# Optimization experiments

Hardware: AMD Instinct MI355X
Metric: run time of the kernel (lower is better)

Reference implementation:

```python
import jax, jax.numpy as jnp
import numpy as np

W = 192      # image width (seq len for attn1)
HN = 192     # H * N (seq len for attn2)
C = 128      # hidden_dim
NHEAD = 8


def setup_inputs() -> dict:
    key = jax.random.key(0)
    ks = jax.random.split(key, 12)
    sc = 0.05  # small init so softmax is well-conditioned
    feat = jax.random.normal(ks[0], (W, 2 * HN, C), jnp.float32)
    pos = jax.random.normal(ks[1], (2 * W - 1, C), jnp.float32)
    pos_y = jax.random.normal(ks[2], (2 * HN - 1, C), jnp.float32)
    i = jnp.arange(W)
    pos_indexes = (i[:, None] - i[None, :] + W - 1).reshape(-1).astype(jnp.int32)
    j = jnp.arange(HN)
    pos_indexes_y = (j[:, None] - j[None, :] + HN - 1).reshape(-1).astype(jnp.int32)
    return {
        "feat": feat,
        "pos": pos,
        "pos_y": pos_y,
        "ln_w": jnp.ones((C,), jnp.float32),
        "ln_b": jnp.zeros((C,), jnp.float32),
        "w_in1": jax.random.normal(ks[3], (3 * C, C), jnp.float32) * sc,
        "b_in1": jnp.zeros((3 * C,), jnp.float32),
        "w_out1": jax.random.normal(ks[4], (C, C), jnp.float32) * sc,
        "b_out1": jnp.zeros((C,), jnp.float32),
        "w_in2": jax.random.normal(ks[5], (3 * C, C), jnp.float32) * sc,
        "b_in2": jnp.zeros((3 * C,), jnp.float32),
        "w_out2": jax.random.normal(ks[6], (C, C), jnp.float32) * sc,
        "b_out2": jnp.zeros((C,), jnp.float32),
        "pos_indexes": pos_indexes,
        "pos_indexes_y": pos_indexes_y,
    }


def _layernorm(x, g, b, eps=1e-5):
    m = x.mean(-1, keepdims=True)
    v = ((x - m) ** 2).mean(-1, keepdims=True)
    return (x - m) / jnp.sqrt(v + eps) * g + b


def _rel_attn(x, pos_enc, pos_idx, w_in, b_in, w_out, b_out):
    # x: [w, bsz, c]; pos_enc: [2w-1, c]; pos_idx: [w*w]
    w, bsz, c = x.shape
    hd = c // NHEAD
    scale = float(hd) ** -0.5
    q, k, v = jnp.split(x @ w_in.T + b_in, 3, axis=-1)
    pe = pos_enc[pos_idx].reshape(w, w, c)           # [w, w, c] relative pos
    q_r, k_r = jnp.split(pe @ w_in[: 2 * c].T + b_in[: 2 * c], 2, axis=-1)
    q = (q * scale).reshape(w, bsz, NHEAD, hd)
    k = k.reshape(w, bsz, NHEAD, hd)
    v = v.reshape(w, bsz, NHEAD, hd)
    q_r = (q_r * scale).reshape(w, w, NHEAD, hd)
    k_r = k_r.reshape(w, w, NHEAD, hd)
    # content-content + content-pos + pos-content -> [bsz, nhead, w, w]
    attn = (jnp.einsum('wnec,vnec->newv', q, k)
            + jnp.einsum('wnec,wvec->newv', q, k_r)
            + jnp.einsum('vnec,wvec->newv', k, q_r))
    attn = jax.nn.softmax(attn, axis=-1)
    out = jnp.einsum('newv,vnec->wnec', attn, v).reshape(w, bsz, c)
    return out @ w_out.T + b_out


def reference(feat, pos, pos_y, ln_w, ln_b,
              w_in1, b_in1, w_out1, b_out1,
              w_in2, b_in2, w_out2, b_out2,
              pos_indexes, pos_indexes_y):
    w, h2, c = feat.shape
    f2 = _layernorm(feat, ln_w, ln_b)
    # [W, 2HN, C] -> [HN, 2W, C]: attention along vertical (H) axis
    f2 = f2.reshape(w, 2, h2 // 2, c).transpose(2, 1, 0, 3).reshape(h2 // 2, 2 * w, c)
    f2 = _rel_attn(f2, pos_y, pos_indexes_y, w_in2, b_in2, w_out2, b_out2)
    # back to [W, 2HN, C]: attention along horizontal (W) axis
    f2 = f2.reshape(h2 // 2, 2, w, c).transpose(2, 1, 0, 3).reshape(w, h2, c)
    f2 = _rel_attn(f2, pos, pos_indexes, w_in1, b_in1, w_out1, b_out1)
    return feat + f2
```

## Files before the change

kernel.cpp:

```cpp
#include <hip/hip_runtime.h>
#include <hip/hip_bf16.h>


typedef unsigned short u16;
typedef short bf16x8 __attribute__((ext_vector_type(8)));
typedef float f32x4 __attribute__((ext_vector_type(4)));
typedef float f32x16 __attribute__((ext_vector_type(16)));

__device__ inline u16 f2bf(float f) {
    union { float f; unsigned u; } a; a.f = f;
    unsigned u = a.u;
    unsigned r = u + 0x7FFFu + ((u >> 16) & 1u);
    return (u16)(r >> 16);
}
__device__ inline unsigned cvt_pk_bf16(float lo, float hi) {
    unsigned r;
    asm("v_cvt_pk_bf16_f32 %0, %1, %2" : "=v"(r) : "v"(lo), "v"(hi));
    return r;
}

__global__ __launch_bounds__(256) void ln_kernel(const float* __restrict__ feat,
                                                 const float* __restrict__ g,
                                                 const float* __restrict__ bta,
                                                 u16* __restrict__ x2) {
    int wid = threadIdx.x >> 6, lane = threadIdx.x & 63;
    int r = blockIdx.x * 4 + wid;
    const float* row = feat + (size_t)r * 128;
    float v0 = row[lane], v1 = row[lane + 64];
    float s = v0 + v1;
    for (int m = 1; m < 64; m <<= 1) s += __shfl_xor(s, m);
    float mean = s * (1.0f / 128.0f);
    float d0 = v0 - mean, d1 = v1 - mean;
    float vs = d0 * d0 + d1 * d1;
    for (int m = 1; m < 64; m <<= 1) vs += __shfl_xor(vs, m);
    float rstd = rsqrtf(vs * (1.0f / 128.0f) + 1e-5f);
    int w = r / 384, rem = r % 384;
    int out_r = (rem % 192) * 384 + (rem / 192) * 192 + w;
    u16* orow = x2 + (size_t)out_r * 128;
    orow[lane]      = f2bf(d0 * rstd * g[lane] + bta[lane]);
    orow[lane + 64] = f2bf(d1 * rstd * g[lane + 64] + bta[lane + 64]);
}

__global__ __launch_bounds__(256) void posproj_kernel(const float* __restrict__ pos,
                                                      const float* __restrict__ w_in,
                                                      const float* __restrict__ b_in,
                                                      u16* __restrict__ qr,
                                                      u16* __restrict__ kr) {
    int d = blockIdx.x, t = threadIdx.x;
    if (d == 383) {
        if (t < 128)      { int e = t >> 4,  j = t & 15;  qr[(e * 384 + 383) * 16 + j] = 0; }
        else              { int t2 = t - 128; int e = t2 >> 4, j = t2 & 15; kr[(e * 384 + 383) * 16 + j] = 0; }
        return;
    }
    __shared__ float prow[128];
    if (t < 128) prow[t] = pos[d * 128 + t];
    __syncthreads();
    const float* wrow = w_in + t * 128;
    float acc = b_in[t];
    #pragma unroll 8
    for (int k = 0; k < 128; ++k) acc += prow[k] * wrow[k];
    int which = t >> 7, e = (t >> 4) & 7, j = t & 15;
    if (which == 0) qr[(e * 384 + d) * 16 + j] = f2bf(acc * 0.25f);
    else            kr[(e * 384 + d) * 16 + j] = f2bf(acc);
}

__global__ __launch_bounds__(256) void qkv_gemm(const u16* __restrict__ X,
                                                const float* __restrict__ Wn,
                                                const float* __restrict__ bias,
                                                u16* __restrict__ Qo,
                                                u16* __restrict__ Ko,
                                                u16* __restrict__ Vo) {
    __shared__ u16 a_lds[128][136];
    __shared__ u16 w_lds[64][136];
    int tid = threadIdx.x;
    int m0 = blockIdx.y * 128, n0 = blockIdx.x * 64;
    #pragma unroll
    for (int i = 0; i < 8; ++i) {
        int idx = tid + 256 * i;
        int row = idx >> 4, c8 = (idx & 15) * 8;
        *(int4*)&a_lds[row][c8] = *(const int4*)&X[(size_t)(m0 + row) * 128 + c8];
    }
    #pragma unroll
    for (int i = 0; i < 8; ++i) {
        int idx = tid + 256 * i;
        int row = idx >> 5, c4 = (idx & 31) * 4;
        float4 f = *(const float4*)&Wn[(size_t)(n0 + row) * 128 + c4];
        uint2 p;
        p.x = (unsigned)f2bf(f.x) | ((unsigned)f2bf(f.y) << 16);
        p.y = (unsigned)f2bf(f.z) | ((unsigned)f2bf(f.w) << 16);
        *(uint2*)&w_lds[row][c4] = p;
    }
    __syncthreads();
    int lane = tid & 63, wid = tid >> 6;
    int wr = (wid >> 1) * 64, wc = (wid & 1) * 32;
    int kg = lane >> 4, l15 = lane & 15;
    f32x4 acc[4][2];
    #pragma unroll
    for (int i = 0; i < 4; ++i)
        #pragma unroll
        for (int j = 0; j < 2; ++j) acc[i][j] = (f32x4){0.f, 0.f, 0.f, 0.f};
    #pragma unroll
    for (int kk = 0; kk < 4; ++kk) {
        int kof = kk * 32 + kg * 8;
        bf16x8 a[4], b[2];
        #pragma unroll
        for (int i = 0; i < 4; ++i) a[i] = *(const bf16x8*)&a_lds[wr + i * 16 + l15][kof];
        #pragma unroll
        for (int j = 0; j < 2; ++j) b[j] = *(const bf16x8*)&w_lds[wc + j * 16 + l15][kof];
        #pragma unroll
        for (int i = 0; i < 4; ++i)
            #pragma unroll
            for (int j = 0; j < 2; ++j)
                acc[i][j] = __builtin_amdgcn_mfma_f32_16x16x32_bf16(a[i], b[j], acc[i][j], 0, 0, 0);
    }
    #pragma unroll
    for (int i = 0; i < 4; ++i)
        #pragma unroll
        for (int j = 0; j < 2; ++j) {
            int col_g = n0 + wc + j * 16 + l15;
            float bv = bias[col_g];
            int which = col_g >> 7, e = (col_g >> 4) & 7, d = col_g & 15;
            u16* dst = which == 0 ? Qo : (which == 1 ? Ko : Vo);
            float scl = which == 0 ? 0.25f : 1.0f;
            #pragma unroll
            for (int ii = 0; ii < 4; ++ii) {
                int row_g = m0 + wr + i * 16 + kg * 4 + ii;
                int batch = row_g % 384, sq = row_g / 384;
                dst[((size_t)(batch * 8 + e) * 192 + sq) * 16 + d] = f2bf((acc[i][j][ii] + bv) * scl);
            }
        }
}

__global__ __launch_bounds__(512, 4) void attn_kernel(const u16* __restrict__ Qg,
                                                      const u16* __restrict__ Kg,
                                                      const u16* __restrict__ Vg,
                                                      const u16* __restrict__ qr_g,
                                                      const u16* __restrict__ kr_g,
                                                      u16* __restrict__ Og) {
    __shared__ float sc[97][100];
    __shared__ u16 Vt[16][200];
    __shared__ float rsum[96];
    int tid = threadIdx.x, lane = tid & 63, wid = tid >> 6;
    int half = blockIdx.x, e = blockIdx.y, b = blockIdx.z;
    int w0 = half * 96;
    size_t base = ((size_t)b * 8 + e) * 192 * 16;

    #pragma unroll
    for (int i = 0; i < 6; ++i) { int idx = tid + 512 * i;
        Vt[idx & 15][idx >> 4] = Vg[base + idx]; }
    if (tid < 96) rsum[tid] = 0.f;
    __syncthreads();

    int lo = lane & 31, hi = lane >> 5, hi8 = hi * 8;
    int l15 = lane & 15, kg = lane >> 4;
    const u16* Qrow  = Qg + base;
    const u16* Krow  = Kg + base;
    const u16* krrow = kr_g + (size_t)e * 384 * 16;
    const u16* qrrow = qr_g + (size_t)e * 384 * 16;
    f32x4 oacc = (f32x4){0.f, 0.f, 0.f, 0.f};

    for (int ch = 0; ch < 2; ++ch) {
        int v0 = ch * 96;

        for (int t = wid; t < 9; t += 8) {
            int wt = t / 3, vt = t % 3;
            bf16x8 ak = *(const bf16x8*)(Krow + (size_t)(v0 + vt * 32 + lo) * 16 + hi8);
            bf16x8 bq = *(const bf16x8*)(Qrow + (size_t)(w0 + wt * 32 + lo) * 16 + hi8);
            f32x16 acc = {};
            acc = __builtin_amdgcn_mfma_f32_32x32x16_bf16(ak, bq, acc, 0, 0, 0);
            float* dst = &sc[wt * 32 + lo][vt * 32 + 4 * hi];
            #pragma unroll
            for (int g = 0; g < 4; ++g) {
                f32x4 vv = { acc[4 * g], acc[4 * g + 1], acc[4 * g + 2], acc[4 * g + 3] };
                *(f32x4*)(dst + 8 * g) = vv;
            }
        }
        __syncthreads();

        for (int t = wid; t < 12; t += 8) {
            int wt = t >> 2, dt = t & 3;
            int D0 = w0 + 32 * wt + 96 - v0 + 32 * dt;
            bf16x8 akr = *(const bf16x8*)(krrow + (size_t)(D0 + lo) * 16 + hi8);
            bf16x8 bq  = *(const bf16x8*)(Qrow + (size_t)(w0 + wt * 32 + lo) * 16 + hi8);
            f32x16 acc = {};
            acc = __builtin_amdgcn_mfma_f32_32x32x16_bf16(akr, bq, acc, 0, 0, 0);
            int row = wt * 32 + lo;
            int cb = lo + 95 - 32 * dt - 4 * hi;
            if (dt == 1 || dt == 2) {
                float* rowp = &sc[row][0];
                #pragma unroll
                for (int ii = 0; ii < 16; ++ii) {
                    const int rr = (ii & 3) + 8 * (ii >> 2);
                    rowp[cb - rr] += acc[ii];
                }
            } else {
                float* rowp = &sc[row][0];
                #pragma unroll
                for (int ii = 0; ii < 16; ++ii) {
                    const int rr = (ii & 3) + 8 * (ii >> 2);
                    int c = cb - rr;
                    int col = ((unsigned)c < 96u) ? c : 96;
                    rowp[col] += acc[ii];
                }
            }
        }
        __syncthreads();

        for (int t = wid; t < 12; t += 8) {
            int vt = t >> 2, dt = t & 3;
            int D0 = w0 - v0 - 32 * vt + 160 + 32 * dt;
            bf16x8 aqr = *(const bf16x8*)(qrrow + (size_t)(D0 + lo) * 16 + hi8);
            bf16x8 bk  = *(const bf16x8*)(Krow + (size_t)(v0 + vt * 32 + lo) * 16 + hi8);
            f32x16 acc = {};
            acc = __builtin_amdgcn_mfma_f32_32x32x16_bf16(aqr, bk, acc, 0, 0, 0);
            int c = vt * 32 + lo;
            int rb = 32 * dt - 31 + lo + 4 * hi;
            if (dt == 1 || dt == 2) {
                #pragma unroll
                for (int ii = 0; ii < 16; ++ii) {
                    const int rr = (ii & 3) + 8 * (ii >> 2);
                    sc[rb + rr][c] += acc[ii];
                }
            } else {
                #pragma unroll
                for (int ii = 0; ii < 16; ++ii) {
                    const int rr = (ii & 3) + 8 * (ii >> 2);
                    int r = rb + rr;
                    int rowi = ((unsigned)r < 96u) ? r : 96;
                    sc[rowi][c] += acc[ii];
                }
            }
        }
        __syncthreads();

        {
            int r = tid >> 2, j = tid & 3;
            if (r < 96) {
                float* srow = &sc[r][j * 24];
                f32x4 X[6];
                #pragma unroll
                for (int k = 0; k < 6; ++k) X[k] = *(const f32x4*)&srow[k * 4];
                float xs[24];
                #pragma unroll
                for (int k = 0; k < 6; ++k) {
                    xs[4 * k]     = __expf(X[k][0]);
                    xs[4 * k + 1] = __expf(X[k][1]);
                    xs[4 * k + 2] = __expf(X[k][2]);
                    xs[4 * k + 3] = __expf(X[k][3]);
                }
                float sum = 0.f;
                #pragma unroll
                for (int k = 0; k < 24; ++k) sum += xs[k];
                f32x4 pkv[3];
                #pragma unroll
                for (int g = 0; g < 3; ++g)
                    #pragma unroll
                    for (int k = 0; k < 4; ++k)
                        pkv[g][k] = __uint_as_float(cvt_pk_bf16(xs[8 * g + 2 * k], xs[8 * g + 2 * k + 1]));
                float* prow = &sc[r][12 * j];
                *(f32x4*)&prow[0] = pkv[0];
                *(f32x4*)&prow[4] = pkv[1];
                *(f32x4*)&prow[8] = pkv[2];
                sum += __shfl_xor(sum, 1);
                sum += __shfl_xor(sum, 2);
                if (j == 0) rsum[r] += sum;
            }
        }
        __syncthreads();

        if (wid < 6) {
            const u16* prow = (const u16*)&sc[wid * 16 + l15][0];
            #pragma unroll
            for (int kt = 0; kt < 3; ++kt) {
                bf16x8 a  = *(const bf16x8*)(prow + kt * 32 + kg * 8);
                bf16x8 bb = *(const bf16x8*)&Vt[l15][v0 + kt * 32 + kg * 8];
                oacc = __builtin_amdgcn_mfma_f32_16x16x32_bf16(a, bb, oacc, 0, 0, 0);
            }
        }
        __syncthreads();
    }

    if (wid < 6) {
        #pragma unroll
        for (int ii = 0; ii < 4; ++ii) {
            int wl = wid * 16 + kg * 4 + ii;
            float val = oacc[ii] * (1.0f / rsum[wl]);
            Og[((size_t)(w0 + wl) * 384 + b) * 128 + e * 16 + l15] = f2bf(val);
        }
    }
}

template <int MODE>
__global__ __launch_bounds__(256) void outproj_gemm(const u16* __restrict__ X,
                                                    const float* __restrict__ Wn,
                                                    const float* __restrict__ bias,
                                                    const float* __restrict__ feat,
                                                    u16* __restrict__ x1o,
                                                    float* __restrict__ outp) {
    __shared__ u16 a_lds[128][136];
    __shared__ u16 w_lds[64][136];
    int tid = threadIdx.x;
    int m0 = blockIdx.y * 128, n0 = blockIdx.x * 64;
    #pragma unroll
    for (int i = 0; i < 8; ++i) {
        int idx = tid + 256 * i;
        int row = idx >> 4, c8 = (idx & 15) * 8;
        *(int4*)&a_lds[row][c8] = *(const int4*)&X[(size_t)(m0 + row) * 128 + c8];
    }
    #pragma unroll
    for (int i = 0; i < 8; ++i) {
        int idx = tid + 256 * i;
        int row = idx >> 5, c4 = (idx & 31) * 4;
        float4 f = *(const float4*)&Wn[(size_t)(n0 + row) * 128 + c4];
        uint2 p;
        p.x = (unsigned)f2bf(f.x) | ((unsigned)f2bf(f.y) << 16);
        p.y = (unsigned)f2bf(f.z) | ((unsigned)f2bf(f.w) << 16);
        *(uint2*)&w_lds[row][c4] = p;
    }
    __syncthreads();
    int lane = tid & 63, wid = tid >> 6;
    int wr = (wid >> 1) * 64, wc = (wid & 1) * 32;
    int kg = lane >> 4, l15 = lane & 15;
    f32x4 acc[4][2];
    #pragma unroll
    for (int i = 0; i < 4; ++i)
        #pragma unroll
        for (int j = 0; j < 2; ++j) acc[i][j] = (f32x4){0.f, 0.f, 0.f, 0.f};
    #pragma unroll
    for (int kk = 0; kk < 4; ++kk) {
        int kof = kk * 32 + kg * 8;
        bf16x8 a[4], b[2];
        #pragma unroll
        for (int i = 0; i < 4; ++i) a[i] = *(const bf16x8*)&a_lds[wr + i * 16 + l15][kof];
        #pragma unroll
        for (int j = 0; j < 2; ++j) b[j] = *(const bf16x8*)&w_lds[wc + j * 16 + l15][kof];
        #pragma unroll
        for (int i = 0; i < 4; ++i)
            #pragma unroll
            for (int j = 0; j < 2; ++j)
                acc[i][j] = __builtin_amdgcn_mfma_f32_16x16x32_bf16(a[i], b[j], acc[i][j], 0, 0, 0);
    }
    #pragma unroll
    for (int i = 0; i < 4; ++i)
        #pragma unroll
        for (int j = 0; j < 2; ++j) {
            int col_g = n0 + wc + j * 16 + l15;
            float bv = bias[col_g];
            #pragma unroll
            for (int ii = 0; ii < 4; ++ii) {
                int row_g = m0 + wr + i * 16 + kg * 4 + ii;
                float val = acc[i][j][ii] + bv;
                if (MODE == 0) {
                    int h = row_g / 384, rem = row_g % 384, s2 = rem / 192, w = rem % 192;
                    x1o[((size_t)(w * 384 + s2 * 192 + h)) * 128 + col_g] = f2bf(val);
                } else {
                    size_t o = (size_t)row_g * 128 + col_g;
                    outp[o] = val + feat[o];
                }
            }
        }
}

extern "C" void kernel_launch(void* const* d_in, const int* in_sizes, int n_in,
                              void* d_out, int out_size, void* d_ws, size_t ws_size,
                              hipStream_t stream) {
    const float* feat   = (const float*)d_in[0];
    const float* pos    = (const float*)d_in[1];
    const float* pos_y  = (const float*)d_in[2];
    const float* ln_w   = (const float*)d_in[3];
    const float* ln_b   = (const float*)d_in[4];
    const float* w_in1  = (const float*)d_in[5];
    const float* b_in1  = (const float*)d_in[6];
    const float* w_out1 = (const float*)d_in[7];
    const float* b_out1 = (const float*)d_in[8];
    const float* w_in2  = (const float*)d_in[9];
    const float* b_in2  = (const float*)d_in[10];
    const float* w_out2 = (const float*)d_in[11];
    const float* b_out2 = (const float*)d_in[12];
    float* out = (float*)d_out;

    char* ws = (char*)d_ws;
    const size_t R = (size_t)73728 * 128;
    u16* x2 = (u16*)ws; ws += R * 2;
    u16* x1 = (u16*)ws; ws += R * 2;
    u16* Q  = (u16*)ws; ws += R * 2;
    u16* K  = (u16*)ws; ws += R * 2;
    u16* V  = (u16*)ws; ws += R * 2;
    u16* O  = (u16*)ws; ws += R * 2;
    u16* qr = (u16*)ws; ws += (size_t)8 * 384 * 16 * 2;
    u16* kr = (u16*)ws; ws += (size_t)8 * 384 * 16 * 2;

    ln_kernel<<<18432, 256, 0, stream>>>(feat, ln_w, ln_b, x2);
    posproj_kernel<<<384, 256, 0, stream>>>(pos_y, w_in2, b_in2, qr, kr);
    qkv_gemm<<<dim3(6, 576), 256, 0, stream>>>(x2, w_in2, b_in2, Q, K, V);
    attn_kernel<<<dim3(2, 8, 384), 512, 0, stream>>>(Q, K, V, qr, kr, O);
    outproj_gemm<0><<<dim3(2, 576), 256, 0, stream>>>(O, w_out2, b_out2, nullptr, x1, nullptr);
    posproj_kernel<<<384, 256, 0, stream>>>(pos, w_in1, b_in1, qr, kr);
    qkv_gemm<<<dim3(6, 576), 256, 0, stream>>>(x1, w_in1, b_in1, Q, K, V);
    attn_kernel<<<dim3(2, 8, 384), 512, 0, stream>>>(Q, K, V, qr, kr, O);
    outproj_gemm<1><<<dim3(2, 576), 256, 0, stream>>>(O, w_out1, b_out1, feat, nullptr, out);
}
```

Before: 436.6 us.

## Retile attention into 64-row blocks of 256 threads and drop redundant barriers

Attention is split into three 64-query-row tiles per (batch, head) using 256-thread blocks instead of two 96-row tiles using 512 threads. In the old layout two of eight waves sat idle in the PV and softmax phases; now every wave has work, and the launch bounds allow more blocks per CU. The sync after the V transpose load is removed. So is the sync between softmax and the PV MFMA, since each wave reads back only the rows it wrote itself. The cost is that the V tile and K data are loaded and transposed three times per head instead of twice.

```diff
diff --git a/kernel.cpp b/kernel.cpp
--- a/kernel.cpp
+++ b/kernel.cpp
@@ -131,25 +131,24 @@
         }
 }
 
-__global__ __launch_bounds__(512, 4) void attn_kernel(const u16* __restrict__ Qg,
+__global__ __launch_bounds__(256, 5) void attn_kernel(const u16* __restrict__ Qg,
                                                       const u16* __restrict__ Kg,
                                                       const u16* __restrict__ Vg,
                                                       const u16* __restrict__ qr_g,
                                                       const u16* __restrict__ kr_g,
                                                       u16* __restrict__ Og) {
-    __shared__ float sc[97][100];
+    __shared__ float sc[65][100];
     __shared__ u16 Vt[16][200];
-    __shared__ float rsum[96];
+    __shared__ float rsum[64];
     int tid = threadIdx.x, lane = tid & 63, wid = tid >> 6;
-    int half = blockIdx.x, e = blockIdx.y, b = blockIdx.z;
-    int w0 = half * 96;
+    int third = blockIdx.x, e = blockIdx.y, b = blockIdx.z;
+    int w0 = third * 64;
     size_t base = ((size_t)b * 8 + e) * 192 * 16;
 
     #pragma unroll
-    for (int i = 0; i < 6; ++i) { int idx = tid + 512 * i;
+    for (int i = 0; i < 12; ++i) { int idx = tid + 256 * i;
         Vt[idx & 15][idx >> 4] = Vg[base + idx]; }
-    if (tid < 96) rsum[tid] = 0.f;
-    __syncthreads();
+    if (tid < 64) rsum[tid] = 0.f;
 
     int lo = lane & 31, hi = lane >> 5, hi8 = hi * 8;
     int l15 = lane & 15, kg = lane >> 4;
@@ -162,7 +161,7 @@
     for (int ch = 0; ch < 2; ++ch) {
         int v0 = ch * 96;
 
-        for (int t = wid; t < 9; t += 8) {
+        for (int t = wid; t < 6; t += 4) {
             int wt = t / 3, vt = t % 3;
             bf16x8 ak = *(const bf16x8*)(Krow + (size_t)(v0 + vt * 32 + lo) * 16 + hi8);
             bf16x8 bq = *(const bf16x8*)(Qrow + (size_t)(w0 + wt * 32 + lo) * 16 + hi8);
@@ -177,45 +176,42 @@
         }
         __syncthreads();
 
-        for (int t = wid; t < 12; t += 8) {
+        for (int t = wid; t < 8; t += 4) {
             int wt = t >> 2, dt = t & 3;
             int D0 = w0 + 32 * wt + 96 - v0 + 32 * dt;
             bf16x8 akr = *(const bf16x8*)(krrow + (size_t)(D0 + lo) * 16 + hi8);
             bf16x8 bq  = *(const bf16x8*)(Qrow + (size_t)(w0 + wt * 32 + lo) * 16 + hi8);
             f32x16 acc = {};
             acc = __builtin_amdgcn_mfma_f32_32x32x16_bf16(akr, bq, acc, 0, 0, 0);
-            int row = wt * 32 + lo;
+            float* rowp = &sc[wt * 32 + lo][0];
             int cb = lo + 95 - 32 * dt - 4 * hi;
             if (dt == 1 || dt == 2) {
-                float* rowp = &sc[row][0];
                 #pragma unroll
                 for (int ii = 0; ii < 16; ++ii) {
                     const int rr = (ii & 3) + 8 * (ii >> 2);
                     rowp[cb - rr] += acc[ii];
                 }
             } else {
-                float* rowp = &sc[row][0];
                 #pragma unroll
                 for (int ii = 0; ii < 16; ++ii) {
                     const int rr = (ii & 3) + 8 * (ii >> 2);
                     int c = cb - rr;
-                    int col = ((unsigned)c < 96u) ? c : 96;
-                    rowp[col] += acc[ii];
+                    rowp[((unsigned)c < 96u) ? c : 96] += acc[ii];
                 }
             }
         }
         __syncthreads();
 
-        for (int t = wid; t < 12; t += 8) {
-            int vt = t >> 2, dt = t & 3;
-            int D0 = w0 - v0 - 32 * vt + 160 + 32 * dt;
+        for (int t = wid; t < 9; t += 4) {
+            int vt = t / 3, dt = t % 3;
+            int D0 = w0 + 160 - v0 - 32 * vt + 32 * dt;
             bf16x8 aqr = *(const bf16x8*)(qrrow + (size_t)(D0 + lo) * 16 + hi8);
             bf16x8 bk  = *(const bf16x8*)(Krow + (size_t)(v0 + vt * 32 + lo) * 16 + hi8);
             f32x16 acc = {};
             acc = __builtin_amdgcn_mfma_f32_32x32x16_bf16(aqr, bk, acc, 0, 0, 0);
             int c = vt * 32 + lo;
             int rb = 32 * dt - 31 + lo + 4 * hi;
-            if (dt == 1 || dt == 2) {
+            if (dt == 1) {
                 #pragma unroll
                 for (int ii = 0; ii < 16; ++ii) {
                     const int rr = (ii & 3) + 8 * (ii >> 2);
@@ -226,8 +222,7 @@
                 for (int ii = 0; ii < 16; ++ii) {
                     const int rr = (ii & 3) + 8 * (ii >> 2);
                     int r = rb + rr;
-                    int rowi = ((unsigned)r < 96u) ? r : 96;
-                    sc[rowi][c] += acc[ii];
+                    sc[((unsigned)r < 64u) ? r : 64][c] += acc[ii];
                 }
             }
         }
@@ -235,40 +230,42 @@
 
         {
             int r = tid >> 2, j = tid & 3;
-            if (r < 96) {
-                float* srow = &sc[r][j * 24];
-                f32x4 X[6];
-                #pragma unroll
-                for (int k = 0; k < 6; ++k) X[k] = *(const f32x4*)&srow[k * 4];
-                float xs[24];
-                #pragma unroll
-                for (int k = 0; k < 6; ++k) {
-                    xs[4 * k]     = __expf(X[k][0]);
-                    xs[4 * k + 1] = __expf(X[k][1]);
-                    xs[4 * k + 2] = __expf(X[k][2]);
-                    xs[4 * k + 3] = __expf(X[k][3]);
-                }
-                float sum = 0.f;
-                #pragma unroll
-                for (int k = 0; k < 24; ++k) sum += xs[k];
-                f32x4 pkv[3];
-                #pragma unroll
-                for (int g = 0; g < 3; ++g)
-                    #pragma unroll
-                    for (int k = 0; k < 4; ++k)
-                        pkv[g][k] = __uint_as_float(cvt_pk_bf16(xs[8 * g + 2 * k], xs[8 * g + 2 * k + 1]));
-                float* prow = &sc[r][12 * j];
-                *(f32x4*)&prow[0] = pkv[0];
-                *(f32x4*)&prow[4] = pkv[1];
-                *(f32x4*)&prow[8] = pkv[2];
-                sum += __shfl_xor(sum, 1);
-                sum += __shfl_xor(sum, 2);
-                if (j == 0) rsum[r] += sum;
-            }
-        }
-        __syncthreads();
-
-        if (wid < 6) {
+            float* srow = &sc[r][j * 24];
+            f32x4 X0 = *(const f32x4*)&srow[0];
+            f32x4 X1 = *(const f32x4*)&srow[4];
+            f32x4 X2 = *(const f32x4*)&srow[8];
+            f32x4 X3 = *(const f32x4*)&srow[12];
+            f32x4 X4 = *(const f32x4*)&srow[16];
+            f32x4 X5 = *(const f32x4*)&srow[20];
+            float xs[24];
+            #pragma unroll
+            for (int k = 0; k < 4; ++k) {
+                xs[k]      = __expf(X0[k]);
+                xs[4 + k]  = __expf(X1[k]);
+                xs[8 + k]  = __expf(X2[k]);
+                xs[12 + k] = __expf(X3[k]);
+                xs[16 + k] = __expf(X4[k]);
+                xs[20 + k] = __expf(X5[k]);
+            }
+            float sum = 0.f;
+            #pragma unroll
+            for (int k = 0; k < 24; ++k) sum += xs[k];
+            f32x4 pkv[3];
+            #pragma unroll
+            for (int g = 0; g < 3; ++g)
+                #pragma unroll
+                for (int k = 0; k < 4; ++k)
+                    pkv[g][k] = __uint_as_float(cvt_pk_bf16(xs[8 * g + 2 * k], xs[8 * g + 2 * k + 1]));
+            float* prow = &sc[r][12 * j];
+            *(f32x4*)&prow[0] = pkv[0];
+            *(f32x4*)&prow[4] = pkv[1];
+            *(f32x4*)&prow[8] = pkv[2];
+            sum += __shfl_xor(sum, 1);
+            sum += __shfl_xor(sum, 2);
+            if (j == 0) rsum[r] += sum;
+        }
+
+        {
             const u16* prow = (const u16*)&sc[wid * 16 + l15][0];
             #pragma unroll
             for (int kt = 0; kt < 3; ++kt) {
@@ -280,13 +277,11 @@
         __syncthreads();
     }
 
-    if (wid < 6) {
-        #pragma unroll
-        for (int ii = 0; ii < 4; ++ii) {
-            int wl = wid * 16 + kg * 4 + ii;
-            float val = oacc[ii] * (1.0f / rsum[wl]);
-            Og[((size_t)(w0 + wl) * 384 + b) * 128 + e * 16 + l15] = f2bf(val);
-        }
+    #pragma unroll
+    for (int ii = 0; ii < 4; ++ii) {
+        int wl = wid * 16 + kg * 4 + ii;
+        float val = oacc[ii] * (1.0f / rsum[wl]);
+        Og[((size_t)(w0 + wl) * 384 + b) * 128 + e * 16 + l15] = f2bf(val);
     }
 }
 
@@ -393,10 +388,10 @@
     ln_kernel<<<18432, 256, 0, stream>>>(feat, ln_w, ln_b, x2);
     posproj_kernel<<<384, 256, 0, stream>>>(pos_y, w_in2, b_in2, qr, kr);
     qkv_gemm<<<dim3(6, 576), 256, 0, stream>>>(x2, w_in2, b_in2, Q, K, V);
-    attn_kernel<<<dim3(2, 8, 384), 512, 0, stream>>>(Q, K, V, qr, kr, O);
+    attn_kernel<<<dim3(3, 8, 384), 256, 0, stream>>>(Q, K, V, qr, kr, O);
     outproj_gemm<0><<<dim3(2, 576), 256, 0, stream>>>(O, w_out2, b_out2, nullptr, x1, nullptr);
     posproj_kernel<<<384, 256, 0, stream>>>(pos, w_in1, b_in1, qr, kr);
     qkv_gemm<<<dim3(6, 576), 256, 0, stream>>>(x1, w_in1, b_in1, Q, K, V);
-    attn_kernel<<<dim3(2, 8, 384), 512, 0, stream>>>(Q, K, V, qr, kr, O);
+    attn_kernel<<<dim3(3, 8, 384), 256, 0, stream>>>(Q, K, V, qr, kr, O);
     outproj_gemm<1><<<dim3(2, 576), 256, 0, stream>>>(O, w_out1, b_out1, feat, nullptr, out);
 }
```

Result: faster. 398.0 us (-8.8%).
